# Optimization experiments

Hardware: AMD Instinct MI355X
Metric: run time of the kernel (lower is better)

Reference implementation:

```python
import jax, jax.numpy as jnp
import numpy as np

EPS = 1e-5
NUM_HEADS = 8
SCALE = 0.125


def _lin_bn_relu(x, w, b, g, beta, mu, var):
    # Linear (y = x @ w.T + b), BatchNorm1d over channel dim (eval-mode affine), ReLU
    y = jnp.einsum('bnc,dc->bnd', x, w) + b
    y = (y - mu) * (g / jnp.sqrt(var + EPS)) + beta
    return jax.nn.relu(y)


def setup_inputs() -> dict:
    key = jax.random.key(0)
    B, N, C = 8, 1024, 512
    keys = jax.random.split(key, 16)
    d = {'x': jax.random.normal(keys[0], (B, N, C), dtype=jnp.float32)}
    for i, p in enumerate(['q', 'k', 'v', 'p']):
        kw, kb, kmu = keys[1 + 3 * i], keys[2 + 3 * i], keys[3 + 3 * i]
        d[f'{p}_w'] = jax.random.normal(kw, (C, C), dtype=jnp.float32) * 0.02
        d[f'{p}_b'] = jnp.zeros((C,), dtype=jnp.float32)
        d[f'{p}_g'] = jnp.ones((C,), dtype=jnp.float32)
        d[f'{p}_beta'] = jnp.zeros((C,), dtype=jnp.float32)
        d[f'{p}_mu'] = jax.random.normal(kmu, (C,), dtype=jnp.float32) * 0.02
        d[f'{p}_var'] = jax.random.uniform(kb, (C,), dtype=jnp.float32, minval=0.5, maxval=1.5)
    return d


def reference(x,
              q_w, q_b, q_g, q_beta, q_mu, q_var,
              k_w, k_b, k_g, k_beta, k_mu, k_var,
              v_w, v_b, v_g, v_beta, v_mu, v_var,
              p_w, p_b, p_g, p_beta, p_mu, p_var):
    B, N, C = x.shape
    H = NUM_HEADS
    dh = C // H

    def heads(t):  # [B,N,C] -> [B,H,N,dh]
        return t.reshape(B, N, H, dh).transpose(0, 2, 1, 3)

    q = heads(_lin_bn_relu(x, q_w, q_b, q_g, q_beta, q_mu, q_var))
    k = heads(_lin_bn_relu(x, k_w, k_b, k_g, k_beta, k_mu, k_var))
    v = heads(_lin_bn_relu(x, v_w, v_b, v_g, v_beta, v_mu, v_var))

    attn = jnp.einsum('bhnd,bhmd->bhnm', q, k) * SCALE  # no softmax
    out = jnp.einsum('bhnm,bhmd->bhnd', attn, v)
    out = out.transpose(0, 2, 1, 3).reshape(B, N, C)
    out = jax.nn.relu(out)  # attn_lif
    return _lin_bn_relu(out, p_w, p_b, p_g, p_beta, p_mu, p_var)
```

## Files before the change

### kernel.cpp

```cpp
#include <hip/hip_runtime.h>


#define CDIM  512
#define NSEQ  1024
#define MROWS 8192

typedef __attribute__((ext_vector_type(8))) __bf16  bf16x8;
typedef __attribute__((ext_vector_type(4))) float   f32x4;
typedef __attribute__((ext_vector_type(8))) ushort  u16x8;

__device__ __forceinline__ float b2f(ushort u) {
    union { uint i; float f; } v; v.i = ((uint)u) << 16; return v.f;
}
__device__ __forceinline__ ushort f2b(float f) {
    union { float f; uint i; } v; v.f = f;
    uint u = v.i;
    u = u + 0x7fffu + ((u >> 16) & 1u);
    return (ushort)(u >> 16);
}
__device__ __forceinline__ float ldv(const void* p, long i, int f32) {
    return f32 ? ((const float*)p)[i] : b2f(((const ushort*)p)[i]);
}

__device__ __forceinline__ void gload16(const void* g, void* l) {
    __builtin_amdgcn_global_load_lds(
        (const __attribute__((address_space(1))) void*)g,
        (__attribute__((address_space(3))) void*)l,
        16, 0, 0);
}

struct BnArgs {
    const void* b[4]; const void* g[4]; const void* be[4];
    const void* mu[4]; const void* va[4];
};
struct WPtrs { const void* w[4]; };

__global__ __launch_bounds__(256) void prep_all(
    const void* __restrict__ x, WPtrs wp, BnArgs bn,
    ushort* __restrict__ Xb, ushort* __restrict__ Wb,
    float* __restrict__ s_all, float* __restrict__ t_all,
    int* __restrict__ flag)
{
    const int blk = blockIdx.x, t = threadIdx.x;

    __shared__ int cnt;
    if (t == 0) cnt = 0;
    __syncthreads();
    {
        const ushort* xu = (const ushort*)x;
        int c = 0;
        for (int i = t; i < 2048; i += 256) {
            uint e = ((uint)xu[i] >> 7) & 0xffu;
            if (e >= 0xC8u) ++c;
        }
        if (c) atomicAdd(&cnt, c);
    }
    __syncthreads();
    const int f32 = cnt > 32;
    if (blk == 0 && t == 0) *flag = f32;

    if (blk < 2048) {
        long i = ((long)blk * 256 + t) * 8;
        if (f32) {
            const float* s = (const float*)x + i;
            u16x8 o;
            #pragma unroll
            for (int j = 0; j < 8; ++j) o[j] = f2b(s[j]);
            *(u16x8*)(Xb + i) = o;
        } else {
            *(u16x8*)(Xb + i) = *(const u16x8*)((const ushort*)x + i);
        }
    } else if (blk < 2560) {
        int bb = blk - 2048;
        int p = bb >> 7;
        long i = ((long)(bb & 127) * 256 + t) * 8;
        const void* src = wp.w[p];
        ushort* d = Wb + (long)p * 262144 + i;
        if (f32) {
            const float* s = (const float*)src + i;
            u16x8 o;
            #pragma unroll
            for (int j = 0; j < 8; ++j) o[j] = f2b(s[j]);
            *(u16x8*)d = o;
        } else {
            *(u16x8*)d = *(const u16x8*)((const ushort*)src + i);
        }
    } else {
        int idx = (blk - 2560) * 256 + t;
        int br = idx >> 9, c = idx & 511;
        float g  = ldv(bn.g[br],  c, f32);
        float be = ldv(bn.be[br], c, f32);
        float mu = ldv(bn.mu[br], c, f32);
        float va = ldv(bn.va[br], c, f32);
        float bb = ldv(bn.b[br],  c, f32);
        float s = g / sqrtf(va + 1e-5f);
        s_all[idx] = s;
        t_all[idx] = (bb - mu) * s + be;
    }
}

__device__ __forceinline__ void gemm128(
    const ushort* __restrict__ A, const ushort* __restrict__ Bw, void* __restrict__ O,
    const float* __restrict__ s_all, const float* __restrict__ t_all,
    int st_off, int of32)
{
    __shared__ ushort As[2][8192];
    __shared__ ushort Bs[2][8192];
    const int t = threadIdx.x;
    const int wave = t >> 6, lane = t & 63;
    const int wr = wave >> 1, wc = wave & 1;
    const long row0 = (long)blockIdx.x * 128;
    const int  col0 = blockIdx.y * 128;

    const ushort* gA = A  + (row0 + (t >> 3)) * CDIM + (t & 7) * 8;
    const ushort* gB = Bw + (long)(col0 + (t >> 3)) * CDIM + (t & 7) * 8;

    auto STAGE = [&](int b, int k0) {
        #pragma unroll
        for (int r = 0; r < 4; ++r) {
            gload16(gA + (long)r * 32 * CDIM + k0, &As[b][r * 2048 + wave * 512]);
            gload16(gB + (long)r * 32 * CDIM + k0, &Bs[b][r * 2048 + wave * 512]);
        }
    };

    f32x4 acc[4][4] = {};

    STAGE(0, 0);
    __syncthreads();

    #pragma unroll
    for (int kt = 0; kt < 8; ++kt) {
        const int cur = kt & 1;
        if (kt < 7) STAGE(cur ^ 1, (kt + 1) * 64);

        #pragma unroll
        for (int ks = 0; ks < 2; ++ks) {
            bf16x8 av[4], bv[4];
            #pragma unroll
            for (int m = 0; m < 4; ++m)
                av[m] = *(const bf16x8*)&As[cur][(wr * 64 + m * 16 + (lane & 15)) * 64 + ks * 32 + (lane >> 4) * 8];
            #pragma unroll
            for (int n = 0; n < 4; ++n)
                bv[n] = *(const bf16x8*)&Bs[cur][(wc * 64 + n * 16 + (lane & 15)) * 64 + ks * 32 + (lane >> 4) * 8];
            #pragma unroll
            for (int m = 0; m < 4; ++m)
                #pragma unroll
                for (int n = 0; n < 4; ++n)
                    acc[m][n] = __builtin_amdgcn_mfma_f32_16x16x32_bf16(av[m], bv[n], acc[m][n], 0, 0, 0);
        }
        __syncthreads();
    }

    const int lr4 = (lane >> 4) * 4, lc = lane & 15;
    #pragma unroll
    for (int n = 0; n < 4; ++n) {
        const int col = col0 + wc * 64 + n * 16 + lc;
        const float s = s_all[st_off + col], tt = t_all[st_off + col];
        #pragma unroll
        for (int m = 0; m < 4; ++m) {
            const long rb = row0 + wr * 64 + m * 16 + lr4;
            #pragma unroll
            for (int i = 0; i < 4; ++i) {
                float v = acc[m][n][i] * s + tt;
                v = v > 0.f ? v : 0.f;
                if (of32) ((float*)O)[(rb + i) * CDIM + col] = v;
                else      ((ushort*)O)[(rb + i) * CDIM + col] = f2b(v);
            }
        }
    }
}

__global__ __launch_bounds__(256) void gemm_qkv(
    const ushort* __restrict__ Xb, const ushort* __restrict__ Wb,
    ushort* __restrict__ QKV,
    const float* __restrict__ s_all, const float* __restrict__ t_all)
{
    int z = blockIdx.z;
    gemm128(Xb, Wb + (long)z * 262144, QKV + (long)z * 4194304,
            s_all, t_all, z * 512, 0);
}

__global__ __launch_bounds__(256) void gemm_p(
    const ushort* __restrict__ Aq, const ushort* __restrict__ Wp,
    void* __restrict__ O,
    const float* __restrict__ s_all, const float* __restrict__ t_all,
    const int* __restrict__ flag)
{
    gemm128(Aq, Wp, O, s_all, t_all, 1536, *flag);
}

__global__ __launch_bounds__(256) void ktv_kernel(
    const ushort* __restrict__ K, const ushort* __restrict__ V,
    float* __restrict__ Spart)
{
    int bh = blockIdx.x, b = bh >> 3, h = bh & 7;
    int ns = blockIdx.y;
    __shared__ float Ks[32][64];
    __shared__ float Vs[32][64];
    int t = threadIdx.x;
    int lr = t >> 3, lc = (t & 7) * 8;
    int r0 = (t >> 4) * 4, c0 = (t & 15) * 4;
    const ushort* Kb = K + ((long)b * NSEQ + ns * 128) * CDIM + h * 64;
    const ushort* Vb = V + ((long)b * NSEQ + ns * 128) * CDIM + h * 64;

    float acc[4][4] = {};
    for (int it = 0; it < 4; ++it) {
        __syncthreads();
        long n = (long)(it * 32 + lr) * CDIM;
        u16x8 kv = *(const u16x8*)&Kb[n + lc];
        u16x8 vv = *(const u16x8*)&Vb[n + lc];
        #pragma unroll
        for (int j = 0; j < 8; ++j) {
            Ks[lr][lc + j] = b2f(kv[j]);
            Vs[lr][lc + j] = b2f(vv[j]);
        }
        __syncthreads();
        #pragma unroll
        for (int nn = 0; nn < 32; ++nn) {
            f32x4 kf = *(const f32x4*)&Ks[nn][r0];
            f32x4 vf = *(const f32x4*)&Vs[nn][c0];
            #pragma unroll
            for (int i = 0; i < 4; ++i)
                #pragma unroll
                for (int j = 0; j < 4; ++j)
                    acc[i][j] += kf[i] * vf[j];
        }
    }
    float* out = Spart + ((long)bh * 8 + ns) * 4096 + r0 * 64 + c0;
    #pragma unroll
    for (int i = 0; i < 4; ++i)
        #pragma unroll
        for (int j = 0; j < 4; ++j)
            out[i * 64 + j] = acc[i][j];
}

__global__ __launch_bounds__(256) void attn_kernel(
    ushort* __restrict__ Q, const float* __restrict__ Spart)
{
    int bh = blockIdx.x, b = bh >> 3, h = bh & 7;
    int m0 = blockIdx.y * 64;
    __shared__ float Ss[64][64];
    __shared__ float Qs[64][68];
    int t = threadIdx.x, ty = t >> 4, tx = t & 15;

    for (int e = t; e < 4096; e += 256) {
        const float* sp = Spart + (long)bh * 32768 + e;
        float v = 0.f;
        #pragma unroll
        for (int ns = 0; ns < 8; ++ns) v += sp[ns * 4096];
        Ss[e >> 6][e & 63] = v;
    }
    ushort* Qb = Q + ((long)(b * NSEQ + m0)) * CDIM + h * 64;
    for (int e = t; e < 4096; e += 256) {
        int r = e >> 6, c = e & 63;
        Qs[c][r] = b2f(Qb[(long)r * CDIM + c]);
    }
    __syncthreads();

    float acc[4][4] = {};
    for (int d1 = 0; d1 < 64; ++d1) {
        f32x4 qv = *(const f32x4*)&Qs[d1][ty * 4];
        f32x4 sv = *(const f32x4*)&Ss[d1][tx * 4];
        #pragma unroll
        for (int i = 0; i < 4; ++i)
            #pragma unroll
            for (int j = 0; j < 4; ++j)
                acc[i][j] += qv[i] * sv[j];
    }
    #pragma unroll
    for (int i = 0; i < 4; ++i) {
        ushort4 o;
        o.x = f2b(fmaxf(0.125f * acc[i][0], 0.f));
        o.y = f2b(fmaxf(0.125f * acc[i][1], 0.f));
        o.z = f2b(fmaxf(0.125f * acc[i][2], 0.f));
        o.w = f2b(fmaxf(0.125f * acc[i][3], 0.f));
        *(ushort4*)&Qb[(long)(ty * 4 + i) * CDIM + tx * 4] = o;
    }
}

extern "C" void kernel_launch(void* const* d_in, const int* in_sizes, int n_in,
                              void* d_out, int out_size, void* d_ws, size_t ws_size,
                              hipStream_t stream)
{
    const void* x = d_in[0];
    WPtrs wp; BnArgs bn;
    for (int p = 0; p < 4; ++p) {
        wp.w[p]   = d_in[1 + 6 * p + 0];
        bn.b[p]   = d_in[1 + 6 * p + 1];
        bn.g[p]   = d_in[1 + 6 * p + 2];
        bn.be[p]  = d_in[1 + 6 * p + 3];
        bn.mu[p]  = d_in[1 + 6 * p + 4];
        bn.va[p]  = d_in[1 + 6 * p + 5];
    }

    char* ws = (char*)d_ws;
    float*  s_all = (float*)ws;
    float*  t_all = (float*)(ws + 8192);
    int*    flag  = (int*)(ws + 16384);
    ushort* Wb    = (ushort*)(ws + 16640);
    ushort* QKV   = (ushort*)(ws + 16640 + 2097152);
    float*  Spart = (float*)(ws + 16640 + 2097152 + 3L * 8388608);
    ushort* Xb    = (ushort*)d_out;

    prep_all<<<2568, 256, 0, stream>>>(x, wp, bn, Xb, Wb, s_all, t_all, flag);

    gemm_qkv<<<dim3(64, 4, 3), 256, 0, stream>>>(Xb, Wb, QKV, s_all, t_all);

    ktv_kernel<<<dim3(64, 8), 256, 0, stream>>>(QKV + 4194304, QKV + 2L * 4194304, Spart);

    attn_kernel<<<dim3(64, 16), 256, 0, stream>>>(QKV, Spart);

    gemm_p<<<dim3(64, 4), 256, 0, stream>>>(QKV, Wb + 3L * 262144, d_out,
                                            s_all, t_all, flag);
}
```

Baseline: 187.3 us.

## Fuse Q·S attention product into projection GEMM and reduce KᵀV via atomics

Removes the separate attention kernel: the projection GEMM now computes each 64x64 head block of relu(scale·Q·S) on the fly with MFMA, stores it to LDS as bf16, and feeds it straight into the Wp GEMM. KᵀV partial sums are accumulated with float atomics into one S buffer, which prep_all zeroes with extra blocks, so there is no 8-way partial reduction. This saves a kernel launch and the round trip of the attention output through global memory. In exchange, S is recomputed per column tile (4x redundant Q·S work), S is rounded to bf16, the atomics add contention, and tiles are smaller at 64 rows.

```diff
diff --git a/kernel.cpp b/kernel.cpp
--- a/kernel.cpp
+++ b/kernel.cpp
@@ -39,9 +39,13 @@
     const void* __restrict__ x, WPtrs wp, BnArgs bn,
     ushort* __restrict__ Xb, ushort* __restrict__ Wb,
     float* __restrict__ s_all, float* __restrict__ t_all,
-    int* __restrict__ flag)
+    float* __restrict__ S, int* __restrict__ flag)
 {
     const int blk = blockIdx.x, t = threadIdx.x;
+    if (blk >= 2568) {
+        ((float4*)S)[(blk - 2568) * 256 + t] = make_float4(0.f, 0.f, 0.f, 0.f);
+        return;
+    }
 
     __shared__ int cnt;
     if (t == 0) cnt = 0;
@@ -180,18 +184,9 @@
             s_all, t_all, z * 512, 0);
 }
 
-__global__ __launch_bounds__(256) void gemm_p(
-    const ushort* __restrict__ Aq, const ushort* __restrict__ Wp,
-    void* __restrict__ O,
-    const float* __restrict__ s_all, const float* __restrict__ t_all,
-    const int* __restrict__ flag)
-{
-    gemm128(Aq, Wp, O, s_all, t_all, 1536, *flag);
-}
-
 __global__ __launch_bounds__(256) void ktv_kernel(
     const ushort* __restrict__ K, const ushort* __restrict__ V,
-    float* __restrict__ Spart)
+    float* __restrict__ S)
 {
     int bh = blockIdx.x, b = bh >> 3, h = bh & 7;
     int ns = blockIdx.y;
@@ -226,55 +221,119 @@
                     acc[i][j] += kf[i] * vf[j];
         }
     }
-    float* out = Spart + ((long)bh * 8 + ns) * 4096 + r0 * 64 + c0;
+    float* out = S + (long)bh * 4096 + r0 * 64 + c0;
     #pragma unroll
     for (int i = 0; i < 4; ++i)
         #pragma unroll
         for (int j = 0; j < 4; ++j)
-            out[i * 64 + j] = acc[i][j];
-}
-
-__global__ __launch_bounds__(256) void attn_kernel(
-    ushort* __restrict__ Q, const float* __restrict__ Spart)
-{
-    int bh = blockIdx.x, b = bh >> 3, h = bh & 7;
-    int m0 = blockIdx.y * 64;
-    __shared__ float Ss[64][64];
-    __shared__ float Qs[64][68];
-    int t = threadIdx.x, ty = t >> 4, tx = t & 15;
-
-    for (int e = t; e < 4096; e += 256) {
-        const float* sp = Spart + (long)bh * 32768 + e;
-        float v = 0.f;
-        #pragma unroll
-        for (int ns = 0; ns < 8; ++ns) v += sp[ns * 4096];
-        Ss[e >> 6][e & 63] = v;
-    }
-    ushort* Qb = Q + ((long)(b * NSEQ + m0)) * CDIM + h * 64;
-    for (int e = t; e < 4096; e += 256) {
-        int r = e >> 6, c = e & 63;
-        Qs[c][r] = b2f(Qb[(long)r * CDIM + c]);
-    }
+            atomicAdd(&out[i * 64 + j], acc[i][j]);
+}
+
+__global__ __launch_bounds__(256) void gemm_p_fused(
+    const ushort* __restrict__ Q, const ushort* __restrict__ Wp,
+    const float* __restrict__ S, void* __restrict__ O,
+    const float* __restrict__ s_all, const float* __restrict__ t_all,
+    const int* __restrict__ flag)
+{
+    __shared__ ushort Qs[2][4096];
+    __shared__ ushort Bs[2][8192];
+    __shared__ ushort St[2][4608];
+    __shared__ ushort As[4096];
+    const int t = threadIdx.x, wave = t >> 6, lane = t & 63;
+    const int wr = wave >> 1, wc = wave & 1;
+    const long row0 = (long)blockIdx.x * 64;
+    const int  col0 = blockIdx.y * 128;
+    const int  b8   = (blockIdx.x >> 4) * 8;
+    const int  of32 = *flag;
+
+    const ushort* gQ = Q  + (row0 + (t >> 3)) * CDIM + (t & 7) * 8;
+    const ushort* gW = Wp + (long)(col0 + (t >> 3)) * CDIM + (t & 7) * 8;
+
+    auto STAGE_Q = [&](int bf, int kt) {
+        #pragma unroll
+        for (int r = 0; r < 2; ++r)
+            gload16(gQ + (long)r * 32 * CDIM + kt * 64, &Qs[bf][r * 2048 + wave * 512]);
+    };
+    auto STAGE_W = [&](int bf, int kt) {
+        #pragma unroll
+        for (int r = 0; r < 4; ++r)
+            gload16(gW + (long)r * 32 * CDIM + kt * 64, &Bs[bf][r * 2048 + wave * 512]);
+    };
+    auto STAGE_S = [&](int bf, int kt) {
+        const float* Sp = S + (long)(b8 + kt) * 4096;
+        #pragma unroll
+        for (int j = 0; j < 16; ++j) {
+            int e = j * 256 + t;
+            St[bf][(e & 63) * 72 + (e >> 6)] = f2b(0.125f * Sp[e]);
+        }
+    };
+
+    f32x4 acc[2][4] = {};
+
+    STAGE_Q(0, 0); STAGE_W(0, 0); STAGE_S(0, 0);
     __syncthreads();
 
-    float acc[4][4] = {};
-    for (int d1 = 0; d1 < 64; ++d1) {
-        f32x4 qv = *(const f32x4*)&Qs[d1][ty * 4];
-        f32x4 sv = *(const f32x4*)&Ss[d1][tx * 4];
-        #pragma unroll
-        for (int i = 0; i < 4; ++i)
-            #pragma unroll
-            for (int j = 0; j < 4; ++j)
-                acc[i][j] += qv[i] * sv[j];
-    }
+    for (int kt = 0; kt < 8; ++kt) {
+        const int cur = kt & 1;
+        if (kt < 7) { STAGE_Q(cur ^ 1, kt + 1); STAGE_W(cur ^ 1, kt + 1); STAGE_S(cur ^ 1, kt + 1); }
+
+        f32x4 p[4] = {};
+        #pragma unroll
+        for (int ks = 0; ks < 2; ++ks) {
+            bf16x8 aq = *(const bf16x8*)&Qs[cur][(wave * 16 + (lane & 15)) * 64 + ks * 32 + (lane >> 4) * 8];
+            #pragma unroll
+            for (int n = 0; n < 4; ++n) {
+                bf16x8 bs = *(const bf16x8*)&St[cur][(n * 16 + (lane & 15)) * 72 + ks * 32 + (lane >> 4) * 8];
+                p[n] = __builtin_amdgcn_mfma_f32_16x16x32_bf16(aq, bs, p[n], 0, 0, 0);
+            }
+        }
+        __syncthreads();
+
+        {
+            const int rb = wave * 16 + (lane >> 4) * 4, cb = lane & 15;
+            #pragma unroll
+            for (int n = 0; n < 4; ++n)
+                #pragma unroll
+                for (int i = 0; i < 4; ++i) {
+                    float v = p[n][i];
+                    As[(rb + i) * 64 + n * 16 + cb] = f2b(v > 0.f ? v : 0.f);
+                }
+        }
+        __syncthreads();
+
+        #pragma unroll
+        for (int ks = 0; ks < 2; ++ks) {
+            bf16x8 av[2], bv[4];
+            #pragma unroll
+            for (int m = 0; m < 2; ++m)
+                av[m] = *(const bf16x8*)&As[(wr * 32 + m * 16 + (lane & 15)) * 64 + ks * 32 + (lane >> 4) * 8];
+            #pragma unroll
+            for (int n = 0; n < 4; ++n)
+                bv[n] = *(const bf16x8*)&Bs[cur][(wc * 64 + n * 16 + (lane & 15)) * 64 + ks * 32 + (lane >> 4) * 8];
+            #pragma unroll
+            for (int m = 0; m < 2; ++m)
+                #pragma unroll
+                for (int n = 0; n < 4; ++n)
+                    acc[m][n] = __builtin_amdgcn_mfma_f32_16x16x32_bf16(av[m], bv[n], acc[m][n], 0, 0, 0);
+        }
+    }
+
+    const int lr4 = (lane >> 4) * 4, lc = lane & 15;
     #pragma unroll
-    for (int i = 0; i < 4; ++i) {
-        ushort4 o;
-        o.x = f2b(fmaxf(0.125f * acc[i][0], 0.f));
-        o.y = f2b(fmaxf(0.125f * acc[i][1], 0.f));
-        o.z = f2b(fmaxf(0.125f * acc[i][2], 0.f));
-        o.w = f2b(fmaxf(0.125f * acc[i][3], 0.f));
-        *(ushort4*)&Qb[(long)(ty * 4 + i) * CDIM + tx * 4] = o;
+    for (int n = 0; n < 4; ++n) {
+        const int col = col0 + wc * 64 + n * 16 + lc;
+        const float s = s_all[1536 + col], tt = t_all[1536 + col];
+        #pragma unroll
+        for (int m = 0; m < 2; ++m) {
+            const long rb = row0 + wr * 32 + m * 16 + lr4;
+            #pragma unroll
+            for (int i = 0; i < 4; ++i) {
+                float v = acc[m][n][i] * s + tt;
+                v = v > 0.f ? v : 0.f;
+                if (of32) ((float*)O)[(rb + i) * CDIM + col] = v;
+                else      ((ushort*)O)[(rb + i) * CDIM + col] = f2b(v);
+            }
+        }
     }
 }
 
@@ -299,17 +358,15 @@
     int*    flag  = (int*)(ws + 16384);
     ushort* Wb    = (ushort*)(ws + 16640);
     ushort* QKV   = (ushort*)(ws + 16640 + 2097152);
-    float*  Spart = (float*)(ws + 16640 + 2097152 + 3L * 8388608);
+    float*  S     = (float*)(ws + 16640 + 2097152 + 3L * 8388608);
     ushort* Xb    = (ushort*)d_out;
 
-    prep_all<<<2568, 256, 0, stream>>>(x, wp, bn, Xb, Wb, s_all, t_all, flag);
+    prep_all<<<2824, 256, 0, stream>>>(x, wp, bn, Xb, Wb, s_all, t_all, S, flag);
 
     gemm_qkv<<<dim3(64, 4, 3), 256, 0, stream>>>(Xb, Wb, QKV, s_all, t_all);
 
-    ktv_kernel<<<dim3(64, 8), 256, 0, stream>>>(QKV + 4194304, QKV + 2L * 4194304, Spart);
-
-    attn_kernel<<<dim3(64, 16), 256, 0, stream>>>(QKV, Spart);
-
-    gemm_p<<<dim3(64, 4), 256, 0, stream>>>(QKV, Wb + 3L * 262144, d_out,
-                                            s_all, t_all, flag);
-}
+    ktv_kernel<<<dim3(64, 8), 256, 0, stream>>>(QKV + 4194304, QKV + 2L * 4194304, S);
+
+    gemm_p_fused<<<dim3(128, 4), 256, 0, stream>>>(QKV, Wb + 3L * 262144, S, d_out,
+                                                   s_all, t_all, flag);
+}
```

New measurement: 207.4 us. 1.11x slower.
